# Kernel tuning notes

Measured on AMD Instinct MI355X. Metric: run time of the kernel, lower is better.

## Reference

```python
import jax, jax.numpy as jnp
import numpy as np

D_MODEL, N_HEAD, D_FF = 768, 12, 3072
HEAD_DIM = D_MODEL // N_HEAD
EPS = 1e-5


def _layernorm(x, g, b):
    mu = jnp.mean(x, axis=-1, keepdims=True)
    var = jnp.mean((x - mu) ** 2, axis=-1, keepdims=True)
    return (x - mu) * jax.lax.rsqrt(var + EPS) * g + b


def setup_inputs() -> dict:
    key = jax.random.key(0)
    ks = jax.random.split(key, 14)
    s = 1.0 / np.sqrt(D_MODEL)
    sf = 1.0 / np.sqrt(D_FF)
    inp = {
        "x": jax.random.normal(ks[0], (2, 2048, D_MODEL), dtype=jnp.float32),
        "Wq": jax.random.normal(ks[1], (D_MODEL, D_MODEL), dtype=jnp.float32) * s,
        "bq": jnp.zeros((D_MODEL,), jnp.float32),
        "Wk": jax.random.normal(ks[2], (D_MODEL, D_MODEL), dtype=jnp.float32) * s,
        "bk": jnp.zeros((D_MODEL,), jnp.float32),
        "Wv": jax.random.normal(ks[3], (D_MODEL, D_MODEL), dtype=jnp.float32) * s,
        "bv": jnp.zeros((D_MODEL,), jnp.float32),
        "Wo": jax.random.normal(ks[4], (D_MODEL, D_MODEL), dtype=jnp.float32) * s,
        "bo": jnp.zeros((D_MODEL,), jnp.float32),
        "W1": jax.random.normal(ks[5], (D_MODEL, D_FF), dtype=jnp.float32) * s,
        "b1": jnp.zeros((D_FF,), jnp.float32),
        "W2": jax.random.normal(ks[6], (D_FF, D_MODEL), dtype=jnp.float32) * sf,
        "b2": jnp.zeros((D_MODEL,), jnp.float32),
        "ln1_g": jnp.ones((D_MODEL,), jnp.float32),
        "ln1_b": jnp.zeros((D_MODEL,), jnp.float32),
        "ln2_g": jnp.ones((D_MODEL,), jnp.float32),
        "ln2_b": jnp.zeros((D_MODEL,), jnp.float32),
    }
    return inp


def reference(x, Wq, bq, Wk, bk, Wv, bv, Wo, bo, W1, b1, W2, b2,
              ln1_g, ln1_b, ln2_g, ln2_b):
    B, S, D = x.shape
    # projections -> [B, H, S, hd]
    def proj(W, b):
        return (x @ W + b).reshape(B, S, N_HEAD, HEAD_DIM).transpose(0, 2, 1, 3)
    q, k, v = proj(Wq, bq), proj(Wk, bk), proj(Wv, bv)
    scores = jnp.einsum("bhqd,bhkd->bhqk", q, k) / jnp.sqrt(
        jnp.asarray(HEAD_DIM, jnp.float32))
    attn = jax.nn.softmax(scores, axis=-1)
    ctx = jnp.einsum("bhqk,bhkd->bhqd", attn, v)
    ctx = ctx.transpose(0, 2, 1, 3).reshape(B, S, D)
    attn_out = ctx @ Wo + bo
    h = _layernorm(x + attn_out, ln1_g, ln1_b)
    ffn = jax.nn.gelu(h @ W1 + b1, approximate=False) @ W2 + b2
    return _layernorm(h + ffn, ln2_g, ln2_b)
```

## Files before the change

### kernel.cpp

```cpp
#include <hip/hip_runtime.h>
#include <hip/hip_bf16.h>
#include <cstdint>
#include <cstddef>

typedef unsigned short u16;
typedef __bf16 bf16x8 __attribute__((ext_vector_type(8)));
typedef float f32x4 __attribute__((ext_vector_type(4)));

#define MFMA_BF16(a, b, c) __builtin_amdgcn_mfma_f32_16x16x32_bf16((a), (b), (c), 0, 0, 0)

#define GLDS16(g, l)                                                        \
  __builtin_amdgcn_global_load_lds(                                         \
      (__attribute__((address_space(1))) void*)(void*)(g),                  \
      (__attribute__((address_space(3))) void*)(void*)(l), 16, 0, 0)

#define QSCALE 0.18033688011112042f
#define PSTRIDE ((size_t)4096 * 768)

__device__ __forceinline__ u16 f2bf(float x) {
  union { float f; unsigned u; } c; c.f = x;
  unsigned u = c.u;
  unsigned r = (u + 0x7fffu + ((u >> 16) & 1u)) >> 16;
  return (u16)r;
}
__device__ __forceinline__ float bf2f(u16 x) {
  union { unsigned u; float f; } c; c.u = (unsigned)x << 16; return c.f;
}

__global__ __launch_bounds__(256) void prep_weights_k(
    const float* __restrict__ Wq, const float* __restrict__ Wk,
    const float* __restrict__ Wv, const float* __restrict__ Wo,
    const float* __restrict__ W1, const float* __restrict__ W2,
    const float* __restrict__ bq, const float* __restrict__ bk,
    const float* __restrict__ bv, const float* __restrict__ x,
    u16* __restrict__ WqkvT, u16* __restrict__ WoT,
    u16* __restrict__ W1T, u16* __restrict__ W2T, float* __restrict__ bqkv,
    u16* __restrict__ xb) {
  const int id = blockIdx.x;
  if (id >= 6921) {
    const int i = ((id - 6921) * 256 + threadIdx.x) * 4;
    const float4 v = *(const float4*)(x + i);
    ushort4 o;
    o.x = f2bf(v.x); o.y = f2bf(v.y); o.z = f2bf(v.z); o.w = f2bf(v.w);
    *(ushort4*)(xb + i) = o;
    return;
  }
  if (id >= 6912) {
    int i = (id - 6912) * 256 + threadIdx.x;
    if (i < 768) bqkv[i] = bq[i];
    else if (i < 1536) bqkv[i] = bk[i - 768];
    else if (i < 2304) bqkv[i] = bv[i - 1536];
    return;
  }
  const float* in; u16* out; int K, N, bx, by;
  if (id < 2304) {
    const int mat = id / 576, t = id - mat * 576;
    in = (mat == 0) ? Wq : (mat == 1) ? Wk : (mat == 2) ? Wv : Wo;
    out = (mat == 0) ? WqkvT : (mat == 1) ? WqkvT + 768 * 768
        : (mat == 2) ? WqkvT + 2 * 768 * 768 : WoT;
    K = 768; N = 768; bx = (t % 24) * 32; by = (t / 24) * 32;
  } else if (id < 4608) {
    const int t = id - 2304;
    in = W1; out = W1T; K = 768; N = 3072;
    bx = (t % 96) * 32; by = (t / 96) * 32;
  } else {
    const int t = id - 4608;
    in = W2; out = W2T; K = 3072; N = 768;
    bx = (t % 24) * 32; by = (t / 24) * 32;
  }
  __shared__ float tile[32][33];
  const int tx = threadIdx.x & 31, ty = threadIdx.x >> 5;
#pragma unroll
  for (int j = 0; j < 32; j += 8)
    tile[ty + j][tx] = in[(size_t)(by + ty + j) * N + bx + tx];
  __syncthreads();
#pragma unroll
  for (int j = 0; j < 32; j += 8)
    out[(size_t)(bx + ty + j) * K + by + tx] = f2bf(tile[tx][ty + j]);
}

template <int EPI>
__global__ __launch_bounds__(256) void gemm_bt(
    const u16* __restrict__ A, const u16* __restrict__ BT,
    const float* __restrict__ bias, int M, int N, int K, int kchunk,
    float* __restrict__ outf, u16* __restrict__ outb,
    u16* __restrict__ qo, u16* __restrict__ ko, u16* __restrict__ vto) {
  __shared__ __align__(16) u16 lsA[2 * 128 * 32];
  __shared__ __align__(16) u16 lsB[2 * 128 * 32];
  const int tid = threadIdx.x;
  const int w = tid >> 6, lane = tid & 63;
  const int wm = w & 1, wn = w >> 1;
  const int lrow = lane & 15, quad = lane >> 4;
  const int m0 = blockIdx.y * 128, n0 = blockIdx.x * 128;
  const int kbeg = blockIdx.z * kchunk;

  f32x4 acc[4][4];
#pragma unroll
  for (int i = 0; i < 4; ++i)
#pragma unroll
    for (int j = 0; j < 4; ++j) acc[i][j] = (f32x4){0.f, 0.f, 0.f, 0.f};

  const int off = tid * 16;
  const int line = tid >> 3;
  const int slotp = tid & 7;
  const int p = slotp ^ (line & 7);
  const int srow = line * 2 + (p >> 2);
  const int scol = (p & 3) * 8;

  const u16* ga0 = A + (size_t)(m0 + srow) * K + scol;
  const u16* gb0 = BT + (size_t)(n0 + srow) * K + scol;

  auto stage = [&](int k0, int buf) {
    char* da = (char*)(lsA + buf * 4096);
    char* db = (char*)(lsB + buf * 4096);
    GLDS16(ga0 + k0, da + off);
    GLDS16(ga0 + k0 + (size_t)64 * K, da + 4096 + off);
    GLDS16(gb0 + k0, db + off);
    GLDS16(gb0 + k0 + (size_t)64 * K, db + 4096 + off);
  };

  const int lline = lrow >> 1;
  const int lslot = (((lrow & 1) << 2) + quad) ^ ((lrow >> 1) & 7);
  const int rdoff = lslot * 8;

  const int niter = kchunk >> 5;
  stage(kbeg, 0);
  for (int t = 0; t < niter; ++t) {
    __syncthreads();
    if (t + 1 < niter) stage(kbeg + (t + 1) * 32, (t + 1) & 1);
    const u16* Ab = lsA + (t & 1) * 4096;
    const u16* Bb = lsB + (t & 1) * 4096;
    bf16x8 af[4], bfr[4];
#pragma unroll
    for (int ms = 0; ms < 4; ++ms)
      af[ms] = *(const bf16x8*)&Ab[(wm * 32 + ms * 8 + lline) * 64 + rdoff];
#pragma unroll
    for (int ns = 0; ns < 4; ++ns)
      bfr[ns] = *(const bf16x8*)&Bb[(wn * 32 + ns * 8 + lline) * 64 + rdoff];
#pragma unroll
    for (int ms = 0; ms < 4; ++ms)
#pragma unroll
      for (int ns = 0; ns < 4; ++ns)
        acc[ms][ns] = MFMA_BF16(af[ms], bfr[ns], acc[ms][ns]);
  }

  u16* const pb = (EPI == 3) ? outb + (size_t)blockIdx.z * PSTRIDE : outb;
#pragma unroll
  for (int ms = 0; ms < 4; ++ms) {
    const int rbase = m0 + wm * 64 + ms * 16 + quad * 4;
#pragma unroll
    for (int ns = 0; ns < 4; ++ns) {
      const int col = n0 + wn * 64 + ns * 16 + lrow;
      if constexpr (EPI == 3) {
#pragma unroll
        for (int r = 0; r < 4; ++r)
          pb[(size_t)(rbase + r) * N + col] = f2bf(acc[ms][ns][r]);
      } else if constexpr (EPI == 2) {
        const float bcol = bias[col];
#pragma unroll
        for (int r = 0; r < 4; ++r) {
          float v = acc[ms][ns][r] + bcol;
          float g = 0.5f * v * (1.0f + erff(v * 0.7071067811865476f));
          outb[(size_t)(rbase + r) * N + col] = f2bf(g);
        }
      } else {
        const float bcol = bias[col];
        const int which = col / 768;
        const int rem = col - which * 768;
        const int hh = rem >> 6, dd = rem & 63;
        const int bI = rbase >> 11, sI = rbase & 2047;
        const size_t bh = (size_t)bI * 12 + hh;
        if (which == 0) {
#pragma unroll
          for (int r = 0; r < 4; ++r)
            qo[(bh * 2048 + sI + r) * 64 + dd] = f2bf((acc[ms][ns][r] + bcol) * QSCALE);
        } else if (which == 1) {
#pragma unroll
          for (int r = 0; r < 4; ++r)
            ko[(bh * 2048 + sI + r) * 64 + dd] = f2bf(acc[ms][ns][r] + bcol);
        } else {
          ushort4 pk;
          pk.x = f2bf(acc[ms][ns][0] + bcol);
          pk.y = f2bf(acc[ms][ns][1] + bcol);
          pk.z = f2bf(acc[ms][ns][2] + bcol);
          pk.w = f2bf(acc[ms][ns][3] + bcol);
          *(ushort4*)(vto + (bh * 64 + dd) * 2048 + sI) = pk;
        }
      }
    }
  }
}

__global__ __launch_bounds__(256) void attn_kernel(
    const u16* __restrict__ q, const u16* __restrict__ k,
    const u16* __restrict__ vT, u16* __restrict__ opart,
    float* __restrict__ lpart) {
  __shared__ __align__(16) u16 lsK[2 * 64 * 64];
  __shared__ __align__(16) u16 lsV[2 * 64 * 64];
  __shared__ __align__(16) u16 lsP[4][32 * 64];
  const int tid = threadIdx.x;
  const int w = tid >> 6, lane = tid & 63;
  const int lrow = lane & 15, quad = lane >> 4;
  const int bh = blockIdx.y;
  const int b = bh / 12, h = bh - b * 12;
  const int q0 = blockIdx.x * 128;
  const int z = blockIdx.z;
  const int kvbeg = z * 1024;

  const u16* qbase = q + (size_t)bh * 2048 * 64;
  const u16* kbase = k + (size_t)bh * 2048 * 64;
  const u16* vbase = vT + (size_t)bh * 64 * 2048;

  bf16x8 qf[2][2];
#pragma unroll
  for (int m = 0; m < 2; ++m) {
    const int qrow = q0 + w * 32 + m * 16 + lrow;
    qf[m][0] = *(const bf16x8*)(qbase + (size_t)qrow * 64 + quad * 8);
    qf[m][1] = *(const bf16x8*)(qbase + (size_t)qrow * 64 + 32 + quad * 8);
  }

  float lsum[2][4] = {{0.f, 0.f, 0.f, 0.f}, {0.f, 0.f, 0.f, 0.f}};
  f32x4 oacc[2][4];
#pragma unroll
  for (int m = 0; m < 2; ++m)
#pragma unroll
    for (int d = 0; d < 4; ++d) oacc[m][d] = (f32x4){0.f, 0.f, 0.f, 0.f};

  const int off = tid * 16;
  const int srow = off >> 7;
  const int schunk = (off >> 4) & 7;
  const int sxc = schunk ^ (srow & 7);
  const int ksrc = srow * 64 + sxc * 8;
  const int vsrc0 = srow * 2048 + sxc * 8;

  const int c0 = quad ^ (lrow & 7);
  const int rd0 = c0 * 8, rd1 = (c0 ^ 4) * 8;

  u16* const lsPw = &lsP[w][0];
  const int jhi_base = lrow >> 3, jlo = lrow & 7;

  auto stage = [&](int kt, int buf) {
    char* dk = (char*)(lsK + buf * 4096);
    char* dv = (char*)(lsV + buf * 4096);
    GLDS16(kbase + (size_t)kt * 64 + ksrc, dk + off);
    GLDS16(kbase + (size_t)(kt + 32) * 64 + ksrc, dk + 4096 + off);
    GLDS16(vbase + vsrc0 + kt, dv + off);
    GLDS16(vbase + vsrc0 + kt + 32 * 2048, dv + 4096 + off);
  };

  stage(kvbeg, 0);
  for (int t = 0; t < 16; ++t) {
    __syncthreads();
    if (t < 15) stage(kvbeg + (t + 1) * 64, (t + 1) & 1);
    const u16* Kb = lsK + (t & 1) * 4096;
    const u16* Vb = lsV + (t & 1) * 4096;

    f32x4 sc[2][4];
#pragma unroll
    for (int ns = 0; ns < 4; ++ns) {
      const u16* kr = Kb + (ns * 16 + lrow) * 64;
      bf16x8 kf0 = *(const bf16x8*)(kr + rd0);
      bf16x8 kf1 = *(const bf16x8*)(kr + rd1);
#pragma unroll
      for (int m = 0; m < 2; ++m) {
        sc[m][ns] = (f32x4){0.f, 0.f, 0.f, 0.f};
        sc[m][ns] = MFMA_BF16(qf[m][0], kf0, sc[m][ns]);
        sc[m][ns] = MFMA_BF16(qf[m][1], kf1, sc[m][ns]);
      }
    }

#pragma unroll
    for (int m = 0; m < 2; ++m)
#pragma unroll
      for (int ns = 0; ns < 4; ++ns) {
        const int jhi = ns * 2 + jhi_base;
#pragma unroll
        for (int r = 0; r < 4; ++r) {
          float p = __builtin_amdgcn_exp2f(sc[m][ns][r]);
          lsum[m][r] += p;
          union { float f; unsigned u; } cv; cv.f = p;
          const int row7 = (quad * 4 + r) & 7;
          lsPw[(m * 16 + quad * 4 + r) * 64 + ((jhi ^ row7) * 8) + jlo] =
              (u16)(cv.u >> 16);
        }
      }

#pragma unroll
    for (int d = 0; d < 4; ++d) {
      const u16* vr = Vb + (d * 16 + lrow) * 64;
      bf16x8 vf0 = *(const bf16x8*)(vr + rd0);
      bf16x8 vf1 = *(const bf16x8*)(vr + rd1);
#pragma unroll
      for (int m = 0; m < 2; ++m) {
        const u16* pr = lsPw + (m * 16 + lrow) * 64;
        bf16x8 pf0 = *(const bf16x8*)(pr + rd0);
        bf16x8 pf1 = *(const bf16x8*)(pr + rd1);
        oacc[m][d] = MFMA_BF16(pf0, vf0, oacc[m][d]);
        oacc[m][d] = MFMA_BF16(pf1, vf1, oacc[m][d]);
      }
    }
  }

#pragma unroll
  for (int m = 0; m < 2; ++m)
#pragma unroll
    for (int r = 0; r < 4; ++r) {
#pragma unroll
      for (int mm = 1; mm <= 8; mm <<= 1)
        lsum[m][r] += __shfl_xor(lsum[m][r], mm);
    }

  u16* const op = opart + (size_t)z * PSTRIDE;
#pragma unroll
  for (int m = 0; m < 2; ++m) {
    const int srow_out = q0 + w * 32 + m * 16 + quad * 4;
#pragma unroll
    for (int d = 0; d < 4; ++d)
#pragma unroll
      for (int r = 0; r < 4; ++r)
        op[(size_t)(b * 2048 + srow_out + r) * 768 + h * 64 + d * 16 + lrow] =
            f2bf(oacc[m][d][r]);
    if (lrow == 0) {
#pragma unroll
      for (int r = 0; r < 4; ++r)
        lpart[(size_t)(z * 24 + bh) * 2048 + srow_out + r] = lsum[m][r];
    }
  }
}

__global__ __launch_bounds__(256) void attn_combine_k(
    const u16* __restrict__ op, const float* __restrict__ lp,
    u16* __restrict__ ctx) {
  const unsigned idx = (blockIdx.x * 256u + threadIdx.x) * 4u;
  const unsigned row = idx / 768u;
  const unsigned c = idx - row * 768u;
  const int b = row >> 11, s = row & 2047;
  const int h = c >> 6;
  const size_t li = (size_t)(b * 12 + h) * 2048 + s;
  const float rinv = 1.f / (lp[li] + lp[(size_t)24 * 2048 + li]);
  ushort4 o0 = *(const ushort4*)(op + idx);
  ushort4 o1 = *(const ushort4*)(op + PSTRIDE + idx);
  ushort4 out;
#define CMB(fld) out.fld = f2bf((bf2f(o0.fld) + bf2f(o1.fld)) * rinv);
  CMB(x) CMB(y) CMB(z) CMB(w)
#undef CMB
  *(ushort4*)(ctx + idx) = out;
}

__global__ __launch_bounds__(256) void ln_kernel(
    const u16* __restrict__ parts, int nparts, const float* __restrict__ bias,
    const float* __restrict__ res, const float* __restrict__ g,
    const float* __restrict__ bb, float* __restrict__ outf, u16* __restrict__ outb) {
  const int row = blockIdx.x;
  const int tid = threadIdx.x;
  const float* pr = res + (size_t)row * 768;
  float v[3], s = 0.f, s2 = 0.f;
#pragma unroll
  for (int j = 0; j < 3; ++j) {
    const int c = tid + j * 256;
    float t = bias[c] + pr[c];
    for (int p = 0; p < nparts; ++p)
      t += bf2f(parts[p * PSTRIDE + (size_t)row * 768 + c]);
    v[j] = t; s += t; s2 += t * t;
  }
#pragma unroll
  for (int m = 32; m > 0; m >>= 1) {
    s += __shfl_xor(s, m);
    s2 += __shfl_xor(s2, m);
  }
  __shared__ float red[8];
  const int w = tid >> 6, lane = tid & 63;
  if (lane == 0) { red[w] = s; red[4 + w] = s2; }
  __syncthreads();
  s = red[0] + red[1] + red[2] + red[3];
  s2 = red[4] + red[5] + red[6] + red[7];
  const float mu = s * (1.f / 768.f);
  const float var = s2 * (1.f / 768.f) - mu * mu;
  const float rstd = rsqrtf(var + 1e-5f);
#pragma unroll
  for (int j = 0; j < 3; ++j) {
    const int c = tid + j * 256;
    const float y = (v[j] - mu) * rstd * g[c] + bb[c];
    if (outf) outf[(size_t)row * 768 + c] = y;
    if (outb) outb[(size_t)row * 768 + c] = f2bf(y);
  }
}

extern "C" void kernel_launch(void* const* d_in, const int* in_sizes, int n_in,
                              void* d_out, int out_size, void* d_ws, size_t ws_size,
                              hipStream_t stream) {
  const float* x    = (const float*)d_in[0];
  const float* Wq   = (const float*)d_in[1];
  const float* bq   = (const float*)d_in[2];
  const float* Wk   = (const float*)d_in[3];
  const float* bk   = (const float*)d_in[4];
  const float* Wv   = (const float*)d_in[5];
  const float* bv   = (const float*)d_in[6];
  const float* Wo   = (const float*)d_in[7];
  const float* bo   = (const float*)d_in[8];
  const float* W1   = (const float*)d_in[9];
  const float* b1   = (const float*)d_in[10];
  const float* W2   = (const float*)d_in[11];
  const float* b2   = (const float*)d_in[12];
  const float* ln1g = (const float*)d_in[13];
  const float* ln1b = (const float*)d_in[14];
  const float* ln2g = (const float*)d_in[15];
  const float* ln2b = (const float*)d_in[16];

  char* ws = (char*)d_ws;
  size_t off = 0;
  auto alloc = [&](size_t bytes) {
    void* p = ws + off;
    off += (bytes + 255) & ~(size_t)255;
    return p;
  };
  u16*  WqkvT = (u16*)alloc(2304ull * 768 * 2);
  u16*  WoT   = (u16*)alloc(768ull * 768 * 2);
  u16*  W1T   = (u16*)alloc(3072ull * 768 * 2);
  u16*  W2T   = (u16*)alloc(768ull * 3072 * 2);
  float* bqkv = (float*)alloc(2304 * 4);
  char* bigbase = (char*)alloc(0);
  u16*  xb    = (u16*)alloc(4096ull * 768 * 2);
  u16*  qb    = (u16*)alloc(24ull * 2048 * 64 * 2);
  u16*  kb    = (u16*)alloc(24ull * 2048 * 64 * 2);
  u16*  vtb   = (u16*)alloc(24ull * 64 * 2048 * 2);
  u16*  ctx   = (u16*)alloc(4096ull * 768 * 2);
  u16*  wop   = (u16*)alloc(2ull * PSTRIDE * 2);
  u16*  opart = wop;
  float* lpart = (float*)alloc(2ull * 24 * 2048 * 4);
  u16*  f2bp  = (u16*)bigbase;
  float* hbuf  = (float*)alloc(4096ull * 768 * 4);
  u16*  hb    = (u16*)alloc(4096ull * 768 * 2);
  u16*  f1    = (u16*)alloc(4096ull * 3072 * 2);

  prep_weights_k<<<9993, 256, 0, stream>>>(Wq, Wk, Wv, Wo, W1, W2, bq, bk, bv, x,
                                           WqkvT, WoT, W1T, W2T, bqkv, xb);

  gemm_bt<0><<<dim3(18, 32, 1), 256, 0, stream>>>(xb, WqkvT, bqkv, 4096, 2304, 768, 768,
                                                  nullptr, nullptr, qb, kb, vtb);
  attn_kernel<<<dim3(16, 24, 2), 256, 0, stream>>>(qb, kb, vtb, opart, lpart);
  attn_combine_k<<<3072, 256, 0, stream>>>(opart, lpart, ctx);
  gemm_bt<3><<<dim3(6, 32, 2), 256, 0, stream>>>(ctx, WoT, nullptr, 4096, 768, 768, 384,
                                                 nullptr, wop, nullptr, nullptr, nullptr);
  ln_kernel<<<4096, 256, 0, stream>>>(wop, 2, bo, x, ln1g, ln1b, hbuf, hb);
  gemm_bt<2><<<dim3(24, 32, 1), 256, 0, stream>>>(hb, W1T, b1, 4096, 3072, 768, 768,
                                                  nullptr, f1, nullptr, nullptr, nullptr);
  gemm_bt<3><<<dim3(6, 32, 4), 256, 0, stream>>>(f1, W2T, nullptr, 4096, 768, 3072, 768,
                                                 nullptr, f2bp, nullptr, nullptr, nullptr);
  ln_kernel<<<4096, 256, 0, stream>>>(f2bp, 4, b2, hbuf, ln2g, ln2b, (float*)d_out, nullptr);
}
```

Baseline: 298.2 us.

## Replace 4-wave 128x128 GEMM blocks with single-wave 64x64 blocks

Rewrites the bf16 GEMM so each block is one wavefront computing a 64x64 tile with its own double-buffered LDS, which removes the block-wide __syncthreads. LDS fragment reads are moved ahead of the next async stage with a sched_barrier to avoid overwriting a live buffer. Grids grow fourfold. Operand reuse across waves is lost, doubling global/L2 traffic per MFMA, and correctness relies on implicit waits for the async LDS loads.

```diff
diff --git a/kernel.cpp b/kernel.cpp
--- a/kernel.cpp
+++ b/kernel.cpp
@@ -80,18 +80,15 @@
 }
 
 template <int EPI>
-__global__ __launch_bounds__(256) void gemm_bt(
+__device__ __forceinline__ void gemm_wave_body(
+    u16* lsA, u16* lsB,
     const u16* __restrict__ A, const u16* __restrict__ BT,
     const float* __restrict__ bias, int M, int N, int K, int kchunk,
-    float* __restrict__ outf, u16* __restrict__ outb,
+    u16* __restrict__ outb,
     u16* __restrict__ qo, u16* __restrict__ ko, u16* __restrict__ vto) {
-  __shared__ __align__(16) u16 lsA[2 * 128 * 32];
-  __shared__ __align__(16) u16 lsB[2 * 128 * 32];
-  const int tid = threadIdx.x;
-  const int w = tid >> 6, lane = tid & 63;
-  const int wm = w & 1, wn = w >> 1;
+  const int lane = threadIdx.x;
   const int lrow = lane & 15, quad = lane >> 4;
-  const int m0 = blockIdx.y * 128, n0 = blockIdx.x * 128;
+  const int m0 = blockIdx.y * 64, n0 = blockIdx.x * 64;
   const int kbeg = blockIdx.z * kchunk;
 
   f32x4 acc[4][4];
@@ -100,43 +97,40 @@
 #pragma unroll
     for (int j = 0; j < 4; ++j) acc[i][j] = (f32x4){0.f, 0.f, 0.f, 0.f};
 
-  const int off = tid * 16;
-  const int line = tid >> 3;
-  const int slotp = tid & 7;
-  const int p = slotp ^ (line & 7);
-  const int srow = line * 2 + (p >> 2);
+  const int g = lane >> 3;
+  const int p = (lane & 7) ^ g;
+  const int rpar = p >> 2;
   const int scol = (p & 3) * 8;
 
-  const u16* ga0 = A + (size_t)(m0 + srow) * K + scol;
-  const u16* gb0 = BT + (size_t)(n0 + srow) * K + scol;
-
   auto stage = [&](int k0, int buf) {
-    char* da = (char*)(lsA + buf * 4096);
-    char* db = (char*)(lsB + buf * 4096);
-    GLDS16(ga0 + k0, da + off);
-    GLDS16(ga0 + k0 + (size_t)64 * K, da + 4096 + off);
-    GLDS16(gb0 + k0, db + off);
-    GLDS16(gb0 + k0 + (size_t)64 * K, db + 4096 + off);
+    char* da = (char*)(lsA + buf * 2048);
+    char* db = (char*)(lsB + buf * 2048);
+#pragma unroll
+    for (int i = 0; i < 4; ++i) {
+      const int row = (i * 8 + g) * 2 + rpar;
+      GLDS16(A + (size_t)(m0 + row) * K + k0 + scol, da + i * 1024 + lane * 16);
+      GLDS16(BT + (size_t)(n0 + row) * K + k0 + scol, db + i * 1024 + lane * 16);
+    }
   };
 
   const int lline = lrow >> 1;
-  const int lslot = (((lrow & 1) << 2) + quad) ^ ((lrow >> 1) & 7);
+  const int lslot = (((lrow & 1) << 2) + quad) ^ lline;
   const int rdoff = lslot * 8;
 
   const int niter = kchunk >> 5;
   stage(kbeg, 0);
   for (int t = 0; t < niter; ++t) {
-    __syncthreads();
+    const u16* Ab = lsA + (t & 1) * 2048;
+    const u16* Bb = lsB + (t & 1) * 2048;
+    bf16x8 af[4], bfr[4];
+#pragma unroll
+    for (int ms = 0; ms < 4; ++ms)
+      af[ms] = *(const bf16x8*)&Ab[(ms * 8 + lline) * 64 + rdoff];
+#pragma unroll
+    for (int ns = 0; ns < 4; ++ns)
+      bfr[ns] = *(const bf16x8*)&Bb[(ns * 8 + lline) * 64 + rdoff];
+    __builtin_amdgcn_sched_barrier(0);
     if (t + 1 < niter) stage(kbeg + (t + 1) * 32, (t + 1) & 1);
-    const u16* Ab = lsA + (t & 1) * 4096;
-    const u16* Bb = lsB + (t & 1) * 4096;
-    bf16x8 af[4], bfr[4];
-#pragma unroll
-    for (int ms = 0; ms < 4; ++ms)
-      af[ms] = *(const bf16x8*)&Ab[(wm * 32 + ms * 8 + lline) * 64 + rdoff];
-#pragma unroll
-    for (int ns = 0; ns < 4; ++ns)
-      bfr[ns] = *(const bf16x8*)&Bb[(wn * 32 + ns * 8 + lline) * 64 + rdoff];
 #pragma unroll
     for (int ms = 0; ms < 4; ++ms)
 #pragma unroll
@@ -147,10 +141,10 @@
   u16* const pb = (EPI == 3) ? outb + (size_t)blockIdx.z * PSTRIDE : outb;
 #pragma unroll
   for (int ms = 0; ms < 4; ++ms) {
-    const int rbase = m0 + wm * 64 + ms * 16 + quad * 4;
+    const int rbase = m0 + ms * 16 + quad * 4;
 #pragma unroll
     for (int ns = 0; ns < 4; ++ns) {
-      const int col = n0 + wn * 64 + ns * 16 + lrow;
+      const int col = n0 + ns * 16 + lrow;
       if constexpr (EPI == 3) {
 #pragma unroll
         for (int r = 0; r < 4; ++r)
@@ -160,8 +154,8 @@
 #pragma unroll
         for (int r = 0; r < 4; ++r) {
           float v = acc[ms][ns][r] + bcol;
-          float g = 0.5f * v * (1.0f + erff(v * 0.7071067811865476f));
-          outb[(size_t)(rbase + r) * N + col] = f2bf(g);
+          float gg = 0.5f * v * (1.0f + erff(v * 0.7071067811865476f));
+          outb[(size_t)(rbase + r) * N + col] = f2bf(gg);
         }
       } else {
         const float bcol = bias[col];
@@ -190,6 +184,23 @@
     }
   }
 }
+
+#define GEMM_WRAP(name, EPI)                                                   \
+  __global__ __launch_bounds__(64) void name(                                  \
+      const u16* __restrict__ A, const u16* __restrict__ BT,                   \
+      const float* __restrict__ bias, int M, int N, int K, int kchunk,         \
+      u16* __restrict__ outb, u16* __restrict__ qo, u16* __restrict__ ko,      \
+      u16* __restrict__ vto) {                                                 \
+    __shared__ __align__(16) u16 lsA[2 * 64 * 32];                             \
+    __shared__ __align__(16) u16 lsB[2 * 64 * 32];                             \
+    gemm_wave_body<EPI>(lsA, lsB, A, BT, bias, M, N, K, kchunk, outb, qo, ko,  \
+                        vto);                                                  \
+  }
+GEMM_WRAP(gemm_qkv_k, 0)
+GEMM_WRAP(gemm_ffn1_k, 2)
+GEMM_WRAP(gemm_wo_k, 3)
+GEMM_WRAP(gemm_ffn2_k, 3)
+#undef GEMM_WRAP
 
 __global__ __launch_bounds__(256) void attn_kernel(
     const u16* __restrict__ q, const u16* __restrict__ k,
@@ -436,16 +447,16 @@
   prep_weights_k<<<9993, 256, 0, stream>>>(Wq, Wk, Wv, Wo, W1, W2, bq, bk, bv, x,
                                            WqkvT, WoT, W1T, W2T, bqkv, xb);
 
-  gemm_bt<0><<<dim3(18, 32, 1), 256, 0, stream>>>(xb, WqkvT, bqkv, 4096, 2304, 768, 768,
-                                                  nullptr, nullptr, qb, kb, vtb);
+  gemm_qkv_k<<<dim3(36, 64, 1), 64, 0, stream>>>(xb, WqkvT, bqkv, 4096, 2304, 768, 768,
+                                                 nullptr, qb, kb, vtb);
   attn_kernel<<<dim3(16, 24, 2), 256, 0, stream>>>(qb, kb, vtb, opart, lpart);
   attn_combine_k<<<3072, 256, 0, stream>>>(opart, lpart, ctx);
-  gemm_bt<3><<<dim3(6, 32, 2), 256, 0, stream>>>(ctx, WoT, nullptr, 4096, 768, 768, 384,
-                                                 nullptr, wop, nullptr, nullptr, nullptr);
+  gemm_wo_k<<<dim3(12, 64, 2), 64, 0, stream>>>(ctx, WoT, nullptr, 4096, 768, 768, 384,
+                                                wop, nullptr, nullptr, nullptr);
   ln_kernel<<<4096, 256, 0, stream>>>(wop, 2, bo, x, ln1g, ln1b, hbuf, hb);
-  gemm_bt<2><<<dim3(24, 32, 1), 256, 0, stream>>>(hb, W1T, b1, 4096, 3072, 768, 768,
-                                                  nullptr, f1, nullptr, nullptr, nullptr);
-  gemm_bt<3><<<dim3(6, 32, 4), 256, 0, stream>>>(f1, W2T, nullptr, 4096, 768, 3072, 768,
-                                                 nullptr, f2bp, nullptr, nullptr, nullptr);
+  gemm_ffn1_k<<<dim3(48, 64, 1), 64, 0, stream>>>(hb, W1T, b1, 4096, 3072, 768, 768,
+                                                  f1, nullptr, nullptr, nullptr);
+  gemm_ffn2_k<<<dim3(12, 64, 4), 64, 0, stream>>>(f1, W2T, nullptr, 4096, 768, 3072, 768,
+                                                  f2bp, nullptr, nullptr, nullptr);
   ln_kernel<<<4096, 256, 0, stream>>>(f2bp, 4, b2, hbuf, ln2g, ln2b, (float*)d_out, nullptr);
 }
```

Result: slower. 351.2 us (+17.8%).
